# Optimization experiments

Hardware: AMD Instinct MI355X
Metric: run time of the kernel (lower is better)

The kernel has to match this reference:

```python
import jax, jax.numpy as jnp
import numpy as np

B, S, D, H = 8, 2048, 1024, 8
CHUNK = D // H
SCALE = float(D) ** (-0.5)  # key_dim ** -0.5, key_dim == num_units here
LN_EPS = 1e-5


def setup_inputs() -> dict:
    key = jax.random.key(0)
    ks = jax.random.split(key, 9)
    s = 0.02
    return {
        "query": jax.random.normal(ks[0], (B, S, D), jnp.float32),
        "keys": jax.random.normal(ks[1], (B, S, D), jnp.float32),
        "Wq": jax.random.normal(ks[2], (D, D), jnp.float32) * s,  # torch Linear weight [out,in]
        "Wk": jax.random.normal(ks[3], (D, D), jnp.float32) * s,
        "Wv": jax.random.normal(ks[4], (D, D), jnp.float32) * s,
        "Wp": jax.random.normal(ks[5], (D, D), jnp.float32) * s,
        "bp": jnp.zeros((D,), jnp.float32),
        "ln_gamma": jnp.ones((D,), jnp.float32),
        "ln_beta": jnp.zeros((D,), jnp.float32),
    }


def reference(query, keys, Wq, Wk, Wv, Wp, bp, ln_gamma, ln_beta):
    # Linear layers (no bias on q/k/v): y = x @ W.T
    Q = jnp.einsum("bsd,ed->bse", query, Wq)
    K = jnp.einsum("bsd,ed->bse", keys, Wk)
    V = jnp.einsum("bsd,ed->bse", keys, Wv)
    # Faithful to original: raw view to [B*h, S, chunk] (no transpose head split)
    Qh = Q.reshape(B * H, S, CHUNK)
    Kh = K.reshape(B * H, S, CHUNK)
    Vh = V.reshape(B * H, S, CHUNK)
    # scores [B*h, S, S], scale, softmax (is_masked=False, dropout_p=0)
    att = jnp.einsum("gqc,gkc->gqk", Qh, Kh) * SCALE
    att = jax.nn.softmax(att, axis=-1)
    ctx = jnp.einsum("gqk,gkc->gqc", att, Vh).reshape(B, S, D)
    # output projection + residual + LayerNorm
    out = jnp.einsum("bsd,ed->bse", ctx, Wp) + bp
    out = out + query
    mu = jnp.mean(out, axis=-1, keepdims=True)
    var = jnp.mean(jnp.square(out - mu), axis=-1, keepdims=True)
    out = (out - mu) * jax.lax.rsqrt(var + LN_EPS) * ln_gamma + ln_beta
    return out
```

## Files before the change

kernel.cpp:

```cpp
#include <hip/hip_runtime.h>

typedef __bf16 bf16x8 __attribute__((ext_vector_type(8)));
typedef float f32x4 __attribute__((ext_vector_type(4)));

#define SCLOG 0.04508422f

__device__ __forceinline__ unsigned short f2bf(float f) {
  union { float f; unsigned int u; } v;
  v.f = f;
  unsigned int u = v.u;
  u += 0x7fffu + ((u >> 16) & 1u);
  return (unsigned short)(u >> 16);
}

__device__ __forceinline__ unsigned asuint(float f) {
  union { float f; unsigned u; } v; v.f = f; return v.u;
}

__device__ __forceinline__ void gld_lds16(const void* g, void* l) {
  __builtin_amdgcn_global_load_lds(
      (const __attribute__((address_space(1))) void*)g,
      (__attribute__((address_space(3))) void*)l, 16, 0, 0);
}

__global__ __launch_bounds__(256) void convert_kernel(
    const float* __restrict__ q, const float* __restrict__ k,
    const float* __restrict__ wq, const float* __restrict__ wk,
    const float* __restrict__ wv, const float* __restrict__ wp,
    unsigned short* __restrict__ qb, unsigned short* __restrict__ kb,
    unsigned short* __restrict__ Wqkv, unsigned short* __restrict__ Wpb) {
  size_t i = (size_t)blockIdx.x * 256 + threadIdx.x;
  const float* src; unsigned short* dst; size_t off;
  if (i < 4194304)      { src = q;  dst = qb;             off = i; }
  else if (i < 8388608) { src = k;  dst = kb;             off = i - 4194304; }
  else if (i < 8650752) { src = wq; dst = Wqkv;           off = i - 8388608; }
  else if (i < 8912896) { src = wk; dst = Wqkv + 1048576; off = i - 8650752; }
  else if (i < 9175040) { src = wv; dst = Wqkv + 2097152; off = i - 8912896; }
  else                  { src = wp; dst = Wpb;            off = i - 9175040; }
  float4 v = ((const float4*)src)[off];
  ushort4 o;
  o.x = f2bf(v.x); o.y = f2bf(v.y); o.z = f2bf(v.z); o.w = f2bf(v.w);
  ((ushort4*)dst)[off] = o;
}

__global__ __launch_bounds__(256) void gemm_qkv_kernel(
    const unsigned short* __restrict__ qb,
    const unsigned short* __restrict__ kb,
    const unsigned short* __restrict__ W,
    unsigned short* __restrict__ Qo,
    unsigned short* __restrict__ Ko,
    unsigned short* __restrict__ Vo) {
  __shared__ unsigned short Alds[128 * 32];
  __shared__ unsigned short Blds[128 * 32];
  const int t   = threadIdx.x;
  const int bid = blockIdx.x;
  const int tn  = bid % 24;
  const int tm  = bid / 24;
  const unsigned short* Aptr = (tn < 8) ? qb : kb;
  const unsigned short* Bptr = W + (size_t)tn * 128 * 1024;

  const int lane = t & 63;
  const int wv   = t >> 6;
  const int wm   = (wv >> 1) * 64;
  const int wn   = (wv & 1) * 64;
  const int fr   = lane & 15;
  const int kq   = (lane >> 4) * 8;

  f32x4 acc[4][4];
#pragma unroll
  for (int i = 0; i < 4; i++)
#pragma unroll
    for (int j = 0; j < 4; j++) acc[i][j] = (f32x4){0.f, 0.f, 0.f, 0.f};

  const int sr = t >> 2;
  const int sc = (t & 3) << 3;
  const unsigned short* gA = Aptr + (size_t)(tm * 128 + sr) * 1024 + sc;
  const unsigned short* gB = Bptr + (size_t)sr * 1024 + sc;
  unsigned short* lA = Alds + t * 8;
  unsigned short* lB = Blds + t * 8;

  for (int k0 = 0; k0 < 1024; k0 += 32) {
    gld_lds16(gA, lA);
    gld_lds16(gA + 64 * 1024, lA + 64 * 32);
    gld_lds16(gB, lB);
    gld_lds16(gB + 64 * 1024, lB + 64 * 32);
    gA += 32; gB += 32;
    __syncthreads();
    bf16x8 af[4], bfr[4];
#pragma unroll
    for (int i = 0; i < 4; i++) {
      af[i]  = *(const bf16x8*)&Alds[(wm + i * 16 + fr) * 32 + kq];
      bfr[i] = *(const bf16x8*)&Blds[(wn + i * 16 + fr) * 32 + kq];
    }
#pragma unroll
    for (int i = 0; i < 4; i++)
#pragma unroll
      for (int j = 0; j < 4; j++)
        acc[i][j] = __builtin_amdgcn_mfma_f32_16x16x32_bf16(af[i], bfr[j], acc[i][j], 0, 0, 0);
    __syncthreads();
  }

  const int sel = tn >> 3;
  unsigned short* Out = sel == 0 ? Qo : (sel == 1 ? Ko : Vo);
  const int ncol0 = tn * 128 - sel * 1024 + wn;
  const int quad = lane >> 4;
  const int cc   = lane & 15;
#pragma unroll
  for (int i = 0; i < 4; i++)
#pragma unroll
    for (int j = 0; j < 4; j++)
#pragma unroll
      for (int r = 0; r < 4; r++) {
        int row = tm * 128 + wm + i * 16 + quad * 4 + r;
        int col = ncol0 + j * 16 + cc;
        Out[(size_t)row * 1024 + col] = f2bf(acc[i][j][r]);
      }
}

__global__ __launch_bounds__(256) void vtrans_kernel(
    const unsigned short* __restrict__ V, unsigned short* __restrict__ Vt) {
  __shared__ unsigned short T[128 * 136];
  const int g  = blockIdx.x >> 4;
  const int kt = blockIdx.x & 15;
  const unsigned short* Vg = V + (size_t)g * 262144 + (size_t)kt * 128 * 128;
  unsigned short* Vtg = Vt + (size_t)g * 262144 + kt * 128;
  const int t = threadIdx.x;
#pragma unroll
  for (int it = 0; it < 8; it++) {
    int seg = t + it * 256;
    int k  = seg >> 4;
    int c8 = (seg & 15) << 3;
    uint4 a = *(const uint4*)(Vg + k * 128 + c8);
    unsigned short* Tp = &T[c8 * 136 + k];
    Tp[0 * 136] = (unsigned short)(a.x & 0xffff);
    Tp[1 * 136] = (unsigned short)(a.x >> 16);
    Tp[2 * 136] = (unsigned short)(a.y & 0xffff);
    Tp[3 * 136] = (unsigned short)(a.y >> 16);
    Tp[4 * 136] = (unsigned short)(a.z & 0xffff);
    Tp[5 * 136] = (unsigned short)(a.z >> 16);
    Tp[6 * 136] = (unsigned short)(a.w & 0xffff);
    Tp[7 * 136] = (unsigned short)(a.w >> 16);
  }
  __syncthreads();
#pragma unroll
  for (int it = 0; it < 8; it++) {
    int seg = t + it * 256;
    int c  = seg >> 4;
    int k8 = (seg & 15) << 3;
    uint4 o = *(const uint4*)&T[c * 136 + k8];
    *(uint4*)(Vtg + (size_t)c * 2048 + k8) = o;
  }
}

__global__ __launch_bounds__(256, 2) void attn_kernel(
    const unsigned short* __restrict__ Q,
    const unsigned short* __restrict__ K,
    const unsigned short* __restrict__ Vt,
    unsigned short* __restrict__ ctx) {
  __shared__ unsigned char smem[81920];
  unsigned char* Psh = smem + 65536;

  const int g  = blockIdx.x >> 4;
  const int qt = blockIdx.x & 15;
  const unsigned short* Qg = Q + (size_t)g * 262144 + (size_t)qt * 16384;
  const unsigned short* Kg = K + (size_t)g * 262144;
  const unsigned short* Vg = Vt + (size_t)g * 262144;

  const int t    = threadIdx.x;
  const int lane = t & 63;
  const int wv   = t >> 6;
  const int fr   = lane & 15;
  const int quad = lane >> 4;

#pragma unroll
  for (int it = 0; it < 8; it++) {
    int seg = t + it * 256;
    int r = seg >> 4, p = seg & 15;
    int c = (p & 8) | ((p ^ r) & 7);
    gld_lds16(Qg + r * 128 + c * 8, smem + seg * 16);
  }
  __syncthreads();
  bf16x8 qf[2][4];
#pragma unroll
  for (int nt = 0; nt < 2; nt++)
#pragma unroll
    for (int kc = 0; kc < 4; kc++) {
      int row = wv * 32 + nt * 16 + fr;
      int c = kc * 4 + quad;
      int p = (c & 8) | ((c ^ (row & 7)) & 7);
      qf[nt][kc] = *(const bf16x8*)(smem + row * 256 + p * 16);
    }
  __syncthreads();

#pragma unroll
  for (int it = 0; it < 4; it++) {
    int seg = t + it * 256;
    int r = seg >> 4, p = seg & 15;
    int c = (p & 8) | ((p ^ r) & 7);
    gld_lds16(Kg + (size_t)r * 128 + c * 8, smem + seg * 16);
  }
#pragma unroll
  for (int it = 0; it < 4; it++) {
    int seg = t + it * 256;
    int r = seg >> 3, p = seg & 7;
    int c = p ^ (r & 7);
    gld_lds16(Vg + (size_t)r * 2048 + c * 8, smem + 32768 + seg * 16);
  }
  __syncthreads();

  f32x4 O[2][8];
#pragma unroll
  for (int qb2 = 0; qb2 < 2; qb2++)
#pragma unroll
    for (int cb = 0; cb < 8; cb++) O[qb2][cb] = (f32x4){0.f, 0.f, 0.f, 0.f};
  float lp[2] = {0.f, 0.f};

#pragma unroll 1
  for (int kt = 0; kt < 32; kt++) {
    unsigned char* Ksh = smem + (unsigned)(kt & 1) * 16384;
    unsigned char* Vsh = smem + 32768 + (unsigned)(kt & 1) * 16384;

    if (kt < 31) {
      unsigned char* Kst = smem + (unsigned)((kt + 1) & 1) * 16384;
      unsigned char* Vst = smem + 32768 + (unsigned)((kt + 1) & 1) * 16384;
#pragma unroll
      for (int it = 0; it < 4; it++) {
        int seg = t + it * 256;
        int r = seg >> 4, p = seg & 15;
        int c = (p & 8) | ((p ^ r) & 7);
        gld_lds16(Kg + (size_t)((kt + 1) * 64 + r) * 128 + c * 8, Kst + seg * 16);
      }
#pragma unroll
      for (int it = 0; it < 4; it++) {
        int seg = t + it * 256;
        int r = seg >> 3, p = seg & 7;
        int c = p ^ (r & 7);
        gld_lds16(Vg + (size_t)r * 2048 + (kt + 1) * 64 + c * 8, Vst + seg * 16);
      }
    }

#pragma unroll
    for (int mt = 0; mt < 4; mt++) {
      bf16x8 kf[4];
#pragma unroll
      for (int kc = 0; kc < 4; kc++) {
        int row = mt * 16 + fr;
        int c = kc * 4 + quad;
        int p = (c & 8) | ((c ^ (row & 7)) & 7);
        kf[kc] = *(const bf16x8*)(Ksh + row * 256 + p * 16);
      }
#pragma unroll
      for (int nt = 0; nt < 2; nt++) {
        f32x4 s = (f32x4){0.f, 0.f, 0.f, 0.f};
#pragma unroll
        for (int kc = 0; kc < 4; kc++)
          s = __builtin_amdgcn_mfma_f32_16x16x32_bf16(kf[kc], qf[nt][kc], s, 0, 0, 0);
        float p0 = exp2f(fminf(s[0] * SCLOG, 30.f));
        float p1 = exp2f(fminf(s[1] * SCLOG, 30.f));
        float p2 = exp2f(fminf(s[2] * SCLOG, 30.f));
        float p3 = exp2f(fminf(s[3] * SCLOG, 30.f));
        lp[nt] += (p0 + p1) + (p2 + p3);
        unsigned u01 = __builtin_amdgcn_perm(asuint(p1) + 0x8000u, asuint(p0) + 0x8000u, 0x07060302u);
        unsigned u23 = __builtin_amdgcn_perm(asuint(p3) + 0x8000u, asuint(p2) + 0x8000u, 0x07060302u);
        int qrow = wv * 32 + nt * 16 + fr;
        int cP = mt * 2 + (quad >> 1);
        int pP = cP ^ (qrow & 7);
        uint2 u2; u2.x = u01; u2.y = u23;
        *(uint2*)(Psh + qrow * 128 + pP * 16 + (quad & 1) * 8) = u2;
      }
    }

    bf16x8 pf[2][2];
#pragma unroll
    for (int qb2 = 0; qb2 < 2; qb2++)
#pragma unroll
      for (int k2 = 0; k2 < 2; k2++) {
        int qrow = wv * 32 + qb2 * 16 + fr;
        int c = k2 * 4 + quad;
        int p = c ^ (qrow & 7);
        pf[qb2][k2] = *(const bf16x8*)(Psh + qrow * 128 + p * 16);
      }
#pragma unroll
    for (int cb = 0; cb < 8; cb++)
#pragma unroll
      for (int k2 = 0; k2 < 2; k2++) {
        int crow = cb * 16 + fr;
        int c = k2 * 4 + quad;
        int p = c ^ (crow & 7);
        bf16x8 vf = *(const bf16x8*)(Vsh + crow * 128 + p * 16);
#pragma unroll
        for (int qb2 = 0; qb2 < 2; qb2++)
          O[qb2][cb] = __builtin_amdgcn_mfma_f32_16x16x32_bf16(pf[qb2][k2], vf, O[qb2][cb], 0, 0, 0);
      }

    __syncthreads();
  }

  float* linv_arr = (float*)(smem + 65536);
#pragma unroll
  for (int nt = 0; nt < 2; nt++) {
    float v = lp[nt];
    v += __shfl_xor(v, 16);
    v += __shfl_xor(v, 32);
    if (quad == 0) linv_arr[wv * 32 + nt * 16 + fr] = 1.f / v;
  }
  unsigned short* Cg = ctx + (size_t)g * 262144 + (size_t)qt * 16384;
#pragma unroll
  for (int qb2 = 0; qb2 < 2; qb2++) {
    float li[4];
#pragma unroll
    for (int r = 0; r < 4; r++) li[r] = linv_arr[wv * 32 + qb2 * 16 + quad * 4 + r];
#pragma unroll
    for (int cb = 0; cb < 8; cb++)
#pragma unroll
      for (int r = 0; r < 4; r++) {
        int qrow = wv * 32 + qb2 * 16 + quad * 4 + r;
        Cg[(size_t)qrow * 128 + cb * 16 + fr] = f2bf(O[qb2][cb][r] * li[r]);
      }
  }
}

__global__ __launch_bounds__(256) void gemm_proj_kernel(
    const unsigned short* __restrict__ A,
    const unsigned short* __restrict__ W,
    const float* __restrict__ bp,
    const float* __restrict__ qres,
    float* __restrict__ out) {
  __shared__ unsigned short Alds[128 * 32];
  __shared__ unsigned short Blds[128 * 32];
  const int t   = threadIdx.x;
  const int bid = blockIdx.x;
  const int tn  = bid % 8;
  const int tm  = bid / 8;
  const unsigned short* Bptr = W + (size_t)tn * 128 * 1024;

  const int lane = t & 63;
  const int wv   = t >> 6;
  const int wm   = (wv >> 1) * 64;
  const int wn   = (wv & 1) * 64;
  const int fr   = lane & 15;
  const int kq   = (lane >> 4) * 8;

  f32x4 acc[4][4];
#pragma unroll
  for (int i = 0; i < 4; i++)
#pragma unroll
    for (int j = 0; j < 4; j++) acc[i][j] = (f32x4){0.f, 0.f, 0.f, 0.f};

  const int sr = t >> 2;
  const int sc = (t & 3) << 3;
  const unsigned short* gA = A + (size_t)(tm * 128 + sr) * 1024 + sc;
  const unsigned short* gB = Bptr + (size_t)sr * 1024 + sc;
  unsigned short* lA = Alds + t * 8;
  unsigned short* lB = Blds + t * 8;

  for (int k0 = 0; k0 < 1024; k0 += 32) {
    gld_lds16(gA, lA);
    gld_lds16(gA + 64 * 1024, lA + 64 * 32);
    gld_lds16(gB, lB);
    gld_lds16(gB + 64 * 1024, lB + 64 * 32);
    gA += 32; gB += 32;
    __syncthreads();
    bf16x8 af[4], bfr[4];
#pragma unroll
    for (int i = 0; i < 4; i++) {
      af[i]  = *(const bf16x8*)&Alds[(wm + i * 16 + fr) * 32 + kq];
      bfr[i] = *(const bf16x8*)&Blds[(wn + i * 16 + fr) * 32 + kq];
    }
#pragma unroll
    for (int i = 0; i < 4; i++)
#pragma unroll
      for (int j = 0; j < 4; j++)
        acc[i][j] = __builtin_amdgcn_mfma_f32_16x16x32_bf16(af[i], bfr[j], acc[i][j], 0, 0, 0);
    __syncthreads();
  }

  const int quad = lane >> 4;
  const int cc   = lane & 15;
#pragma unroll
  for (int i = 0; i < 4; i++)
#pragma unroll
    for (int j = 0; j < 4; j++)
#pragma unroll
      for (int r = 0; r < 4; r++) {
        int row = tm * 128 + wm + i * 16 + quad * 4 + r;
        int col = tn * 128 + wn + j * 16 + cc;
        out[(size_t)row * 1024 + col] =
            acc[i][j][r] + bp[col] + qres[(size_t)row * 1024 + col];
      }
}

__global__ __launch_bounds__(256) void ln_kernel(float* __restrict__ out,
                                                 const float* __restrict__ gamma,
                                                 const float* __restrict__ beta) {
  __shared__ float red[8];
  const int row = blockIdx.x;
  float* p = out + (size_t)row * 1024;
  const int t = threadIdx.x;
  float4 v = ((const float4*)p)[t];
  float s  = v.x + v.y + v.z + v.w;
  float s2 = v.x * v.x + v.y * v.y + v.z * v.z + v.w * v.w;
#pragma unroll
  for (int off = 1; off < 64; off <<= 1) {
    s  += __shfl_xor(s, off);
    s2 += __shfl_xor(s2, off);
  }
  const int wv = t >> 6;
  if ((t & 63) == 0) { red[wv] = s; red[4 + wv] = s2; }
  __syncthreads();
  float S  = red[0] + red[1] + red[2] + red[3];
  float S2 = red[4] + red[5] + red[6] + red[7];
  float mu  = S * (1.f / 1024.f);
  float var = S2 * (1.f / 1024.f) - mu * mu;
  float rstd = rsqrtf(var + 1e-5f);
  float4 gm = ((const float4*)gamma)[t];
  float4 bt = ((const float4*)beta)[t];
  v.x = (v.x - mu) * rstd * gm.x + bt.x;
  v.y = (v.y - mu) * rstd * gm.y + bt.y;
  v.z = (v.z - mu) * rstd * gm.z + bt.z;
  v.w = (v.w - mu) * rstd * gm.w + bt.w;
  ((float4*)p)[t] = v;
}

extern "C" void kernel_launch(void* const* d_in, const int* in_sizes, int n_in,
                              void* d_out, int out_size, void* d_ws, size_t ws_size,
                              hipStream_t stream) {
  const float* query = (const float*)d_in[0];
  const float* keys  = (const float*)d_in[1];
  const float* Wq    = (const float*)d_in[2];
  const float* Wk    = (const float*)d_in[3];
  const float* Wv    = (const float*)d_in[4];
  const float* Wp    = (const float*)d_in[5];
  const float* bp    = (const float*)d_in[6];
  const float* gamma = (const float*)d_in[7];
  const float* beta  = (const float*)d_in[8];
  float* out = (float*)d_out;

  unsigned short* ws   = (unsigned short*)d_ws;
  unsigned short* qb   = ws;
  unsigned short* kb   = ws + 16777216;
  unsigned short* Wqkv = ws + 33554432;
  unsigned short* Wpb  = ws + 36700160;
  unsigned short* Qb   = ws + 37748736;
  unsigned short* Kb   = ws + 54525952;
  unsigned short* Vb   = ws + 71303168;
  unsigned short* Vtb  = kb;
  unsigned short* ctx  = qb;

  convert_kernel<<<36864, 256, 0, stream>>>(query, keys, Wq, Wk, Wv, Wp, qb, kb, Wqkv, Wpb);
  gemm_qkv_kernel<<<3072, 256, 0, stream>>>(qb, kb, Wqkv, Qb, Kb, Vb);
  vtrans_kernel<<<1024, 256, 0, stream>>>(Vb, Vtb);
  attn_kernel<<<1024, 256, 0, stream>>>(Qb, Kb, Vtb, ctx);
  gemm_proj_kernel<<<1024, 256, 0, stream>>>(ctx, Wpb, bp, query, out);
  ln_kernel<<<16384, 256, 0, stream>>>(out, gamma, beta);
}
```

Measured before the change: 599.8 us.

## Rewrite QKV GEMM with 256x256 tiles, double-buffered swizzled LDS and 8 waves

Replaces the 128x128, 4-wave QKV projection GEMM with a 256x256 tile, 8-wave kernel. It uses a K-step of 64 held in a double-buffered 128KB LDS ring with XOR swizzling, prefetches via global_load_lds while interleaving MFMA phases with barriers and s_setprio, and remaps blocks for L2 locality. The goal is more data reuse per LDS load, hiding global latency behind compute and avoiding bank conflicts. In exchange it needs heavy LDS and register use, which caps occupancy, and it relies on fragile hand-placed waitcnt and barrier scheduling.

```diff
diff --git a/kernel.cpp b/kernel.cpp
--- a/kernel.cpp
+++ b/kernel.cpp
@@ -43,78 +43,141 @@
   ((ushort4*)dst)[off] = o;
 }
 
-__global__ __launch_bounds__(256) void gemm_qkv_kernel(
+#define QKV_BAR __builtin_amdgcn_s_barrier()
+#define QKV_LGKM asm volatile("s_waitcnt lgkmcnt(0)" ::: "memory")
+
+#define QKV_STG(lc, h, srcb, s)                                               \
+  gld_lds16((srcb) + (size_t)(s) * 128 + gro0, (lc) + (h) * 16384 + d0);      \
+  gld_lds16((srcb) + (size_t)(s) * 128 + gro1, (lc) + (h) * 16384 + d0 + 1024);
+
+#define QKV_RDA(I0)                                                           \
+  _Pragma("unroll") for (int i4 = 0; i4 < 4; ++i4) {                          \
+    af[i4][0] = *(const bf16x8*)(tb + rbA + ((I0) + i4) * 2048 + cx0);        \
+    af[i4][1] = *(const bf16x8*)(tb + rbA + ((I0) + i4) * 2048 + cx1);        \
+  }
+
+#define QKV_RDB(JP)                                                           \
+  _Pragma("unroll") for (int j2 = 0; j2 < 2; ++j2) {                          \
+    bfr[JP][j2][0] = *(const bf16x8*)(tb + rbB + ((JP) * 2 + j2) * 2048 + cx0); \
+    bfr[JP][j2][1] = *(const bf16x8*)(tb + rbB + ((JP) * 2 + j2) * 2048 + cx1); \
+  }
+
+#define QKV_MM(I0, JP)                                                        \
+  _Pragma("unroll") for (int i4 = 0; i4 < 4; ++i4)                            \
+  _Pragma("unroll") for (int j2 = 0; j2 < 2; ++j2)                            \
+  _Pragma("unroll") for (int kk = 0; kk < 2; ++kk)                            \
+    acc[(I0) + i4][(JP) * 2 + j2] = __builtin_amdgcn_mfma_f32_16x16x32_bf16(  \
+        af[i4][kk], bfr[JP][j2][kk], acc[(I0) + i4][(JP) * 2 + j2], 0, 0, 0);
+
+__global__ __launch_bounds__(512, 2) void gemm_qkv8_kernel(
     const unsigned short* __restrict__ qb,
     const unsigned short* __restrict__ kb,
     const unsigned short* __restrict__ W,
     unsigned short* __restrict__ Qo,
     unsigned short* __restrict__ Ko,
     unsigned short* __restrict__ Vo) {
-  __shared__ unsigned short Alds[128 * 32];
-  __shared__ unsigned short Blds[128 * 32];
-  const int t   = threadIdx.x;
-  const int bid = blockIdx.x;
-  const int tn  = bid % 24;
-  const int tm  = bid / 24;
-  const unsigned short* Aptr = (tn < 8) ? qb : kb;
-  const unsigned short* Bptr = W + (size_t)tn * 128 * 1024;
-
+  __shared__ char lds[131072];
+
+  const int t = threadIdx.x;
   const int lane = t & 63;
-  const int wv   = t >> 6;
-  const int wm   = (wv >> 1) * 64;
-  const int wn   = (wv & 1) * 64;
-  const int fr   = lane & 15;
-  const int kq   = (lane >> 4) * 8;
-
-  f32x4 acc[4][4];
-#pragma unroll
-  for (int i = 0; i < 4; i++)
-#pragma unroll
-    for (int j = 0; j < 4; j++) acc[i][j] = (f32x4){0.f, 0.f, 0.f, 0.f};
-
-  const int sr = t >> 2;
-  const int sc = (t & 3) << 3;
-  const unsigned short* gA = Aptr + (size_t)(tm * 128 + sr) * 1024 + sc;
-  const unsigned short* gB = Bptr + (size_t)sr * 1024 + sc;
-  unsigned short* lA = Alds + t * 8;
-  unsigned short* lB = Blds + t * 8;
-
-  for (int k0 = 0; k0 < 1024; k0 += 32) {
-    gld_lds16(gA, lA);
-    gld_lds16(gA + 64 * 1024, lA + 64 * 32);
-    gld_lds16(gB, lB);
-    gld_lds16(gB + 64 * 1024, lB + 64 * 32);
-    gA += 32; gB += 32;
-    __syncthreads();
-    bf16x8 af[4], bfr[4];
-#pragma unroll
-    for (int i = 0; i < 4; i++) {
-      af[i]  = *(const bf16x8*)&Alds[(wm + i * 16 + fr) * 32 + kq];
-      bfr[i] = *(const bf16x8*)&Blds[(wn + i * 16 + fr) * 32 + kq];
+  const int w = t >> 6;
+  const int fr = lane & 15;
+  const int quad = lane >> 4;
+
+  const int orig = blockIdx.x;
+  const int sseq = orig >> 3;
+  const int tn = sseq >> 3;
+  const int tm = (orig & 7) * 8 + (sseq & 7);
+
+  const unsigned short* Ap = (tn < 4) ? qb : kb;
+  const char* aBase = (const char*)Ap + (size_t)(tm * 256) * 2048;
+  const char* bBase = (const char*)W + (size_t)(tn * 256) * 2048;
+
+  const int wm2 = w >> 2, wn4 = w & 3;
+
+  const size_t gro0 = (size_t)(w * 16 + (lane >> 3)) * 2048 + (size_t)(((lane & 7) ^ (lane >> 3)) << 4);
+  const size_t gro1 = gro0 + 8 * 2048;
+  const int d0 = w * 2048 + lane * 16;
+
+  const int rbA = (wm2 * 128 + fr) * 128;
+  const int rbB = 32768 + (wn4 * 64 + fr) * 128;
+  const int cx0 = (quad * 16) ^ ((fr & 7) << 4);
+  const int cx1 = cx0 ^ 64;
+
+  f32x4 acc[8][4];
+#pragma unroll
+  for (int i = 0; i < 8; ++i)
+#pragma unroll
+    for (int j = 0; j < 4; ++j) acc[i][j] = (f32x4){0.f, 0.f, 0.f, 0.f};
+
+#pragma unroll
+  for (int s = 0; s < 2; ++s) {
+    char* lc = lds + s * 65536;
+    QKV_STG(lc, 0, aBase, s);
+    QKV_STG(lc, 1, aBase + 262144, s);
+    QKV_STG(lc + 32768, 0, bBase, s);
+    QKV_STG(lc + 32768, 1, bBase + 262144, s);
+  }
+  asm volatile("s_waitcnt vmcnt(8)" ::: "memory");
+  QKV_BAR;
+
+#pragma unroll 1
+  for (int kt = 0; kt < 16; ++kt) {
+    const char* tb = lds + (kt & 1) * 65536;
+    char* lc = lds + (kt & 1) * 65536;
+    const int s = kt + 2;
+    bf16x8 af[4][2], bfr[2][2][2];
+
+    QKV_RDA(0);
+    QKV_RDB(0);
+    QKV_BAR; QKV_LGKM;
+    __builtin_amdgcn_s_setprio(1);
+    QKV_MM(0, 0);
+    __builtin_amdgcn_s_setprio(0);
+    QKV_BAR;
+
+    QKV_RDB(1);
+    QKV_BAR; QKV_LGKM;
+    __builtin_amdgcn_s_setprio(1);
+    QKV_MM(0, 1);
+    __builtin_amdgcn_s_setprio(0);
+    QKV_BAR;
+
+    QKV_RDA(4);
+    if (s < 16) {
+      QKV_STG(lc + 32768, 0, bBase, s);
+      QKV_STG(lc + 32768, 1, bBase + 262144, s);
     }
-#pragma unroll
-    for (int i = 0; i < 4; i++)
-#pragma unroll
-      for (int j = 0; j < 4; j++)
-        acc[i][j] = __builtin_amdgcn_mfma_f32_16x16x32_bf16(af[i], bfr[j], acc[i][j], 0, 0, 0);
-    __syncthreads();
-  }
-
-  const int sel = tn >> 3;
+    QKV_BAR; QKV_LGKM;
+    __builtin_amdgcn_s_setprio(1);
+    QKV_MM(4, 1);
+    __builtin_amdgcn_s_setprio(0);
+    QKV_BAR;
+
+    if (s < 16) {
+      QKV_STG(lc, 0, aBase, s);
+      QKV_STG(lc, 1, aBase + 262144, s);
+    }
+    QKV_BAR;
+    __builtin_amdgcn_s_setprio(1);
+    QKV_MM(4, 0);
+    __builtin_amdgcn_s_setprio(0);
+    if (kt <= 13)      { asm volatile("s_waitcnt vmcnt(8)" ::: "memory"); }
+    else if (kt == 14) { asm volatile("s_waitcnt vmcnt(0)" ::: "memory"); }
+    if (kt < 15) QKV_BAR;
+  }
+
+  const int sel = tn >> 2;
   unsigned short* Out = sel == 0 ? Qo : (sel == 1 ? Ko : Vo);
-  const int ncol0 = tn * 128 - sel * 1024 + wn;
-  const int quad = lane >> 4;
-  const int cc   = lane & 15;
-#pragma unroll
-  for (int i = 0; i < 4; i++)
-#pragma unroll
-    for (int j = 0; j < 4; j++)
-#pragma unroll
-      for (int r = 0; r < 4; r++) {
-        int row = tm * 128 + wm + i * 16 + quad * 4 + r;
-        int col = ncol0 + j * 16 + cc;
-        Out[(size_t)row * 1024 + col] = f2bf(acc[i][j][r]);
-      }
+  const int row0 = tm * 256 + wm2 * 128 + quad * 4;
+  const int col0 = (tn & 3) * 256 + wn4 * 64 + fr;
+#pragma unroll
+  for (int i = 0; i < 8; ++i)
+#pragma unroll
+    for (int j = 0; j < 4; ++j)
+#pragma unroll
+      for (int r = 0; r < 4; ++r)
+        Out[(size_t)(row0 + i * 16 + r) * 1024 + col0 + j * 16] = f2bf(acc[i][j][r]);
 }
 
 __global__ __launch_bounds__(256) void vtrans_kernel(
@@ -448,7 +511,7 @@
   unsigned short* ctx  = qb;
 
   convert_kernel<<<36864, 256, 0, stream>>>(query, keys, Wq, Wk, Wv, Wp, qb, kb, Wqkv, Wpb);
-  gemm_qkv_kernel<<<3072, 256, 0, stream>>>(qb, kb, Wqkv, Qb, Kb, Vb);
+  gemm_qkv8_kernel<<<768, 512, 0, stream>>>(qb, kb, Wqkv, Qb, Kb, Vb);
   vtrans_kernel<<<1024, 256, 0, stream>>>(Vb, Vtb);
   attn_kernel<<<1024, 256, 0, stream>>>(Qb, Kb, Vtb, ctx);
   gemm_proj_kernel<<<1024, 256, 0, stream>>>(ctx, Wpb, bp, query, out);
```

New measurement: 565.4 us. 1.06x faster.
